# Kernel tuning notes

Hardware: AMD Instinct MI355X
Metric: run time of the kernel (lower is better)

Reference implementation:

```python
import jax, jax.numpy as jnp
import numpy as np

S, D, H = 2048, 1024, 16
DH = D // H
EPS = 1e-5


def setup_inputs() -> dict:
    key = jax.random.key(0)
    ks = jax.random.split(key, 6)
    scale = 0.02
    return {
        "inputs": jax.random.normal(ks[0], (S, D), dtype=jnp.float32),
        "ln_w": jnp.ones((D,), dtype=jnp.float32),
        "ln_b": jnp.zeros((D,), dtype=jnp.float32),
        "Wq": jax.random.normal(ks[1], (D, D), dtype=jnp.float32) * scale,
        "Wk": jax.random.normal(ks[2], (D, D), dtype=jnp.float32) * scale,
        "Wv": jax.random.normal(ks[3], (D, D), dtype=jnp.float32) * scale,
        "Wo": jax.random.normal(ks[4], (D, D), dtype=jnp.float32) * scale,
    }


def reference(inputs, ln_w, ln_b, Wq, Wk, Wv, Wo):
    # Pre-LayerNorm (per token), matching eqx.nn.LayerNorm (eps=1e-5)
    mu = jnp.mean(inputs, axis=-1, keepdims=True)
    var = jnp.var(inputs, axis=-1, keepdims=True)
    x = (inputs - mu) / jnp.sqrt(var + EPS) * ln_w + ln_b  # [S, D]

    # QKV projections (eqx Linear: y = W @ x, no bias) -> [S, H, DH]
    q = (x @ Wq.T).reshape(S, H, DH)
    k = (x @ Wk.T).reshape(S, H, DH)
    v = (x @ Wv.T).reshape(S, H, DH)

    # Scaled dot-product attention; softmax forced to full precision
    scores = jnp.einsum("shd,thd->hst", q, k) / jnp.sqrt(jnp.asarray(DH, x.dtype))
    attn = jax.nn.softmax(scores.astype(jnp.float32), axis=-1).astype(x.dtype)
    # (dropout is identity in inference mode)
    ctx = jnp.einsum("hst,thd->shd", attn, v).reshape(S, D)

    out = ctx @ Wo.T  # output projection
    # outer dropout is identity in inference mode; residual add
    return out + inputs
```

## Files before the change

### kernel.cpp

```cpp
#include <hip/hip_runtime.h>
#include <cstdint>
#include <cstddef>

typedef unsigned short u16;
typedef unsigned int u32;
typedef __attribute__((ext_vector_type(8))) short bf16x8;
typedef __attribute__((ext_vector_type(4))) short bf16x4;
typedef __attribute__((ext_vector_type(4))) float f32x4;
typedef __attribute__((ext_vector_type(4))) unsigned short u16x4;

#if __has_builtin(__builtin_amdgcn_mfma_f32_16x16x16bf16_1k)
#define MFMA16(a, b, c) __builtin_amdgcn_mfma_f32_16x16x16bf16_1k(a, b, c, 0, 0, 0)
#else
static __device__ __forceinline__ f32x4 mfma16_asm(bf16x4 a, bf16x4 b, f32x4 c) {
  asm volatile("v_mfma_f32_16x16x16_bf16 %0, %1, %2, %0\n\ts_nop 4"
               : "+v"(c) : "v"(a), "v"(b));
  return c;
}
#define MFMA16(a, b, c) mfma16_asm(a, b, c)
#endif

__device__ __forceinline__ u16 f2b(float f) {
  union { float f; unsigned u; } un; un.f = f;
  unsigned u = un.u;
  return (u16)((u + 0x7fffu + ((u >> 16) & 1u)) >> 16);
}

__device__ __forceinline__ u32 pkbf(float a, float b) {
  union { float f; u32 u; } ua, ub; ua.f = a; ub.f = b;
  return ((ua.u + 0x8000u) >> 16) | (((ub.u + 0x8000u) >> 16) << 16);
}

__device__ __forceinline__ void gload_lds16(const u16* g, u16* l) {
  __builtin_amdgcn_global_load_lds(
      (const __attribute__((address_space(1))) void*)g,
      (__attribute__((address_space(3))) void*)l, 16, 0, 0);
}

__device__ __forceinline__ void gemm128x64(
    const u16* __restrict__ A, const u16* __restrict__ B,
    u16* smA, u16* smB, int bm, int bn,
    float* outf, u16* outb, const float* __restrict__ resid, int ostride)
{
  const int tid = threadIdx.x;
  const int wave = tid >> 6, lane = tid & 63;
  const int quad = lane >> 4, l16 = lane & 15;
  const int wm = wave >> 1, wn = wave & 1;

  f32x4 acc[4][2];
  const f32x4 zero4 = {0.f, 0.f, 0.f, 0.f};
#pragma unroll
  for (int i = 0; i < 4; i++)
#pragma unroll
    for (int j = 0; j < 2; j++) acc[i][j] = zero4;

  for (int k0 = 0; k0 < 1024; k0 += 32) {
#pragma unroll
    for (int r = 0; r < 2; r++) {
      const int c = r * 256 + wave * 64 + lane;
      gload_lds16(A + (size_t)(bm * 128 + (c >> 2)) * 1024 + k0 + (c & 3) * 8,
                  smA + (size_t)(r * 256 + wave * 64) * 8);
    }
    {
      const int c = wave * 64 + lane;
      gload_lds16(B + (size_t)(bn * 64 + (c >> 2)) * 1024 + k0 + (c & 3) * 8,
                  smB + (size_t)(wave * 64) * 8);
    }
    __syncthreads();
    bf16x8 afr[4], bfr[2];
#pragma unroll
    for (int t = 0; t < 4; t++)
      afr[t] = *(const bf16x8*)(smA + (wm * 64 + t * 16 + l16) * 32 + quad * 8);
#pragma unroll
    for (int t = 0; t < 2; t++)
      bfr[t] = *(const bf16x8*)(smB + (wn * 32 + t * 16 + l16) * 32 + quad * 8);
#pragma unroll
    for (int mt = 0; mt < 4; mt++)
#pragma unroll
      for (int nt = 0; nt < 2; nt++)
        acc[mt][nt] = __builtin_amdgcn_mfma_f32_16x16x32_bf16(afr[mt], bfr[nt], acc[mt][nt], 0, 0, 0);
    __syncthreads();
  }
#pragma unroll
  for (int mt = 0; mt < 4; mt++)
#pragma unroll
    for (int nt = 0; nt < 2; nt++)
#pragma unroll
      for (int r = 0; r < 4; r++) {
        const int row = bm * 128 + wm * 64 + mt * 16 + quad * 4 + r;
        const int col = bn * 64 + wn * 32 + nt * 16 + l16;
        if (outb) outb[(size_t)row * ostride + col] = f2b(acc[mt][nt][r]);
        else outf[(size_t)row * ostride + col] =
                 acc[mt][nt][r] + resid[(size_t)row * ostride + col];
      }
}

__global__ __launch_bounds__(256, 3) void proj_k(
    const u16* __restrict__ xb, const u16* __restrict__ Wb,
    u16* __restrict__ qkbuf, u16* __restrict__ vTb)
{
  __shared__ u16 smA[128 * 32];
  __shared__ u16 smB[64 * 32];
  int b = blockIdx.x;
  const u16 *A, *B; u16* o; int bm, bn;
  if (b < 512) {
    A = xb; B = Wb; o = qkbuf; bm = b >> 5; bn = b & 31;
  } else {
    b -= 512;
    A = Wb + (size_t)2 * (1 << 20); B = xb; o = vTb; bm = b >> 5; bn = b & 31;
  }
  gemm128x64(A, B, smA, smB, bm, bn, nullptr, o, nullptr, 2048);
}

__global__ __launch_bounds__(256, 3) void out_k(
    const u16* __restrict__ ctxb, const u16* __restrict__ Wob,
    float* __restrict__ out, const float* __restrict__ x)
{
  __shared__ u16 smA[128 * 32];
  __shared__ u16 smB[64 * 32];
  gemm128x64(ctxb, Wob, smA, smB, blockIdx.y, blockIdx.x, out, nullptr, x, 1024);
}

__global__ __launch_bounds__(256) void pre_k(
    const float* __restrict__ x, const float* __restrict__ lnw, const float* __restrict__ lnb,
    const float* __restrict__ w0, const float* __restrict__ w1,
    const float* __restrict__ w2, const float* __restrict__ w3,
    u16* __restrict__ xb, u16* __restrict__ Wb)
{
  const int b = blockIdx.x;
  const int tid = threadIdx.x;
  if (b < 2048) {
    const int s = b;
    const float4 v = ((const float4*)(x + (size_t)s * 1024))[tid];
    float sum = v.x + v.y + v.z + v.w;
    float sq  = v.x * v.x + v.y * v.y + v.z * v.z + v.w * v.w;
#pragma unroll
    for (int off = 32; off >= 1; off >>= 1) {
      sum += __shfl_down(sum, off);
      sq  += __shfl_down(sq, off);
    }
    __shared__ float sS[4], sQ[4];
    const int wave = tid >> 6, lane = tid & 63;
    if (lane == 0) { sS[wave] = sum; sQ[wave] = sq; }
    __syncthreads();
    const float ts = sS[0] + sS[1] + sS[2] + sS[3];
    const float tq = sQ[0] + sQ[1] + sQ[2] + sQ[3];
    const float mu = ts * (1.0f / 1024.0f);
    const float var = tq * (1.0f / 1024.0f) - mu * mu;
    const float rstd = rsqrtf(var + 1e-5f);
    const float4 wv = ((const float4*)lnw)[tid];
    const float4 bv = ((const float4*)lnb)[tid];
    u16x4 o;
    o[0] = f2b((v.x - mu) * rstd * wv.x + bv.x);
    o[1] = f2b((v.y - mu) * rstd * wv.y + bv.y);
    o[2] = f2b((v.z - mu) * rstd * wv.z + bv.z);
    o[3] = f2b((v.w - mu) * rstd * wv.w + bv.w);
    *(u16x4*)(xb + (size_t)s * 1024 + tid * 4) = o;
  } else {
    const unsigned i = (unsigned)(b - 2048) * 1024u + tid * 4u;
    const unsigned NW = 1u << 20;
    const float* src; unsigned loc; float sc;
    if (i < NW)            { src = w0; loc = i;           sc = 0.125f; }
    else if (i < 2u * NW)  { src = w1; loc = i - NW;      sc = 1.0f; }
    else if (i < 3u * NW)  { src = w2; loc = i - 2u * NW; sc = 1.0f; }
    else                   { src = w3; loc = i - 3u * NW; sc = 1.0f; }
    const float4 v = *(const float4*)(src + loc);
    u16x4 r;
    r[0] = f2b(v.x * sc); r[1] = f2b(v.y * sc); r[2] = f2b(v.z * sc); r[3] = f2b(v.w * sc);
    *(u16x4*)(Wb + i) = r;
  }
}

__global__ __launch_bounds__(256, 2) void attn_k(
    const u16* __restrict__ qkbuf,
    const u16* __restrict__ vT,
    u16* __restrict__ ctx)
{
  const int h = blockIdx.y;
  const int q0 = blockIdx.x * 64;
  __shared__ __align__(16) unsigned char arena[65536];
  u16* kvbuf = (u16*)arena;
  const int tid = threadIdx.x;
  const int wave = tid >> 6, lane = tid & 63;
  const int quad = lane >> 4, l16 = lane & 15;
  const int a7 = l16 & 7;
  const u16* kg = qkbuf + 1024;

  bf16x8 qf[4][2];
#pragma unroll
  for (int s = 0; s < 4; s++)
#pragma unroll
    for (int ks = 0; ks < 2; ks++)
      qf[s][ks] = *(const bf16x8*)(qkbuf + (size_t)(q0 + s * 16 + l16) * 2048 + h * 64 + ks * 32 + quad * 8);

  const f32x4 zero4 = {0.f, 0.f, 0.f, 0.f};
  f32x4 Oacc[4][4];
#pragma unroll
  for (int s = 0; s < 4; s++)
#pragma unroll
    for (int dt = 0; dt < 4; dt++) Oacc[s][dt] = zero4;
  float lacc[4] = {0.f, 0.f, 0.f, 0.f};

#define STAGE(T, bf)                                                                     \
  {                                                                                      \
    _Pragma("unroll")                                                                    \
    for (int i = 0; i < 4; i++) {                                                        \
      const int idx = (wave * 4 + i) * 64 + lane;                                        \
      const int kt = idx >> 3, kc = (idx & 7) ^ (kt & 7);                                \
      gload_lds16(kg + (size_t)((T) * 128 + kt) * 2048 + h * 64 + kc * 8,                \
                  kvbuf + (bf) * 16384 + (size_t)(wave * 4 + i) * 512);                  \
      const int vd = idx >> 4, vc = (idx & 15) ^ (vd & 7);                               \
      gload_lds16(vT + (size_t)(h * 64 + vd) * 2048 + (T) * 128 + vc * 8,                \
                  kvbuf + (bf) * 16384 + 8192 + (size_t)(wave * 4 + i) * 512);           \
    }                                                                                    \
  }

  STAGE(0, 0);
  __syncthreads();

  for (int T = 0; T < 16; T++) {
    const int bf = T & 1;
    if (T + 1 < 16) STAGE(T + 1, 1 - bf);
    const u16* kb = kvbuf + bf * 16384;
    const u16* vb = kb + 8192;

    f32x4 st[2][4];
#pragma unroll
    for (int ntl = 0; ntl < 2; ntl++) {
      const int nt = wave * 2 + ntl;
      const u16* kr = kb + (nt * 16 + l16) * 64;
      const bf16x8 ka0 = *(const bf16x8*)(kr + (quad ^ a7) * 8);
      const bf16x8 ka1 = *(const bf16x8*)(kr + ((4 + quad) ^ a7) * 8);
#pragma unroll
      for (int s = 0; s < 4; s++) {
        f32x4 t0 = __builtin_amdgcn_mfma_f32_16x16x32_bf16(ka0, qf[s][0], zero4, 0, 0, 0);
        st[ntl][s] = __builtin_amdgcn_mfma_f32_16x16x32_bf16(ka1, qf[s][1], t0, 0, 0, 0);
      }
    }

    bf16x4 pk[2][4];
#pragma unroll
    for (int ntl = 0; ntl < 2; ntl++)
#pragma unroll
      for (int s = 0; s < 4; s++) {
        const float p0 = __expf(st[ntl][s][0]);
        const float p1 = __expf(st[ntl][s][1]);
        const float p2 = __expf(st[ntl][s][2]);
        const float p3 = __expf(st[ntl][s][3]);
        lacc[s] += (p0 + p1) + (p2 + p3);
        union { u32 u[2]; bf16x4 v; } pp;
        pp.u[0] = pkbf(p0, p1);
        pp.u[1] = pkbf(p2, p3);
        pk[ntl][s] = pp.v;
      }

#pragma unroll
    for (int ntl = 0; ntl < 2; ntl++)
#pragma unroll
      for (int dt = 0; dt < 4; dt++) {
        const bf16x4 bv = *(const bf16x4*)(vb + (dt * 16 + l16) * 128 +
            (((wave * 4 + ntl * 2 + (quad >> 1)) ^ a7) * 8 + (quad & 1) * 4));
#pragma unroll
        for (int s = 0; s < 4; s++)
          Oacc[s][dt] = MFMA16(pk[ntl][s], bv, Oacc[s][dt]);
      }
    __syncthreads();
  }
#undef STAGE

  float* rl = (float*)arena;
#pragma unroll
  for (int s = 0; s < 4; s++) {
    float l = lacc[s];
    l += __shfl_xor(l, 16);
    l += __shfl_xor(l, 32);
    if (quad == 0) rl[wave * 64 + s * 16 + l16] = l;
  }
  __syncthreads();
  const int m = tid >> 2, dg = (tid & 3) * 16;
  const float inv = 1.0f / (rl[m] + rl[64 + m] + rl[128 + m] + rl[192 + m]);
  __syncthreads();

  float* ro = (float*)arena;
#pragma unroll
  for (int s = 0; s < 4; s++)
#pragma unroll
    for (int dt = 0; dt < 4; dt++)
#pragma unroll
      for (int r = 0; r < 4; r++) {
        const int mr = s * 16 + quad * 4 + r;
        const int dc = (dt * 16 + l16) ^ ((mr & 7) << 1);
        ro[wave * 4096 + mr * 64 + dc] = Oacc[s][dt][r];
      }
  __syncthreads();
  u16* dst = ctx + (size_t)(q0 + m) * 1024 + h * 64 + dg;
  const int msw = (m & 7) << 1;
#pragma unroll
  for (int g = 0; g < 4; g++) {
    u16x4 o;
#pragma unroll
    for (int j = 0; j < 4; j++) {
      const int dc = (dg + g * 4 + j) ^ msw;
      const int base = m * 64 + dc;
      const float v = ro[base] + ro[4096 + base] + ro[8192 + base] + ro[12288 + base];
      o[j] = f2b(v * inv);
    }
    *(u16x4*)(dst + g * 4) = o;
  }
}

extern "C" void kernel_launch(void* const* d_in, const int* in_sizes, int n_in,
                              void* d_out, int out_size, void* d_ws, size_t ws_size,
                              hipStream_t stream)
{
  const float* x   = (const float*)d_in[0];
  const float* lnw = (const float*)d_in[1];
  const float* lnb = (const float*)d_in[2];
  const float* Wq  = (const float*)d_in[3];
  const float* Wk  = (const float*)d_in[4];
  const float* Wv  = (const float*)d_in[5];
  const float* Wo  = (const float*)d_in[6];

  u16* ws    = (u16*)d_ws;
  u16* xb    = ws;
  u16* Wb    = xb + (size_t)2048 * 1024;
  u16* qkbuf = Wb + (size_t)4 * 1024 * 1024;
  u16* vTb   = qkbuf + (size_t)2048 * 2048;
  u16* ctxb  = vTb + (size_t)1024 * 2048;

  pre_k<<<6144, 256, 0, stream>>>(x, lnw, lnb, Wq, Wk, Wv, Wo, xb, Wb);
  proj_k<<<768, 256, 0, stream>>>(xb, Wb, qkbuf, vTb);
  attn_k<<<dim3(32, 16), 256, 0, stream>>>(qkbuf, vTb, ctxb);
  out_k<<<dim3(16, 16), 256, 0, stream>>>(ctxb, Wb + (size_t)3 * (1 << 20), (float*)d_out, x);
}
```

Before: 153.3 us.

## Give each wave private LDS staging and drop block-wide barriers in GEMMs and attention

The GEMM and attention kernels now have each wave load only the A/B or K/V tiles it consumes into its own LDS region. Each wave waits on its own vmcnt and no longer hits __syncthreads every k-step. Fragments are read to registers before the next stage is issued, so a single double buffer is safe without barriers. The Q scale now folds in log2(e) so exp2f replaces __expf. The cost is that shared tiles are loaded once per wave instead of once per block, which raises global traffic and LDS use, and out_k occupancy drops from 3 to 2 blocks.

```diff
diff --git a/kernel.cpp b/kernel.cpp
--- a/kernel.cpp
+++ b/kernel.cpp
@@ -20,6 +20,8 @@
 #define MFMA16(a, b, c) mfma16_asm(a, b, c)
 #endif
 
+#define VMWAIT0() asm volatile("s_waitcnt vmcnt(0)" ::: "memory")
+
 __device__ __forceinline__ u16 f2b(float f) {
   union { float f; unsigned u; } un; un.f = f;
   unsigned u = un.u;
@@ -37,88 +39,113 @@
       (__attribute__((address_space(3))) void*)l, 16, 0, 0);
 }
 
-__device__ __forceinline__ void gemm128x64(
-    const u16* __restrict__ A, const u16* __restrict__ B,
-    u16* smA, u16* smB, int bm, int bn,
-    float* outf, u16* outb, const float* __restrict__ resid, int ostride)
-{
+#define GEMM_STAGE(ks, bfi)                                                               \
+  {                                                                                       \
+    const int k0g = (ks) * 32;                                                            \
+    u16* ad = (u16*)(wbase + (bfi) * 4096);                                               \
+    u16* bd = (u16*)(wbase + 8192 + (bfi) * 2048);                                        \
+    _Pragma("unroll")                                                                     \
+    for (int i = 0; i < 4; i++)                                                           \
+      gload_lds16(Ag + (size_t)(am0 + i * 16 + (lane >> 2)) * 1024 + k0g + (lane & 3) * 8,\
+                  ad + i * 512);                                                          \
+    _Pragma("unroll")                                                                     \
+    for (int i = 0; i < 2; i++)                                                           \
+      gload_lds16(Bg + (size_t)(bn0 + i * 16 + (lane >> 2)) * 1024 + k0g + (lane & 3) * 8,\
+                  bd + i * 512);                                                          \
+  }
+
+#define GEMM_BODY()                                                                       \
+  f32x4 acc[4][2];                                                                        \
+  {                                                                                       \
+    const f32x4 zero4 = {0.f, 0.f, 0.f, 0.f};                                             \
+    _Pragma("unroll")                                                                     \
+    for (int i = 0; i < 4; i++)                                                           \
+      _Pragma("unroll")                                                                   \
+      for (int j = 0; j < 2; j++) acc[i][j] = zero4;                                      \
+  }                                                                                       \
+  GEMM_STAGE(0, 0);                                                                       \
+  for (int ks = 0; ks < 32; ks++) {                                                       \
+    const int bfi = ks & 1;                                                               \
+    const u16* aw = (const u16*)(wbase + bfi * 4096);                                     \
+    const u16* bw = (const u16*)(wbase + 8192 + bfi * 2048);                              \
+    VMWAIT0();                                                                            \
+    bf16x8 afr[4], bfr[2];                                                                \
+    _Pragma("unroll")                                                                     \
+    for (int t = 0; t < 4; t++)                                                           \
+      afr[t] = *(const bf16x8*)(aw + (t * 16 + l16) * 32 + quad * 8);                     \
+    _Pragma("unroll")                                                                     \
+    for (int t = 0; t < 2; t++)                                                           \
+      bfr[t] = *(const bf16x8*)(bw + (t * 16 + l16) * 32 + quad * 8);                     \
+    if (ks + 1 < 32) GEMM_STAGE(ks + 1, 1 - bfi);                                         \
+    _Pragma("unroll")                                                                     \
+    for (int mt = 0; mt < 4; mt++)                                                        \
+      _Pragma("unroll")                                                                   \
+      for (int nt = 0; nt < 2; nt++)                                                      \
+        acc[mt][nt] = __builtin_amdgcn_mfma_f32_16x16x32_bf16(afr[mt], bfr[nt],           \
+                                                              acc[mt][nt], 0, 0, 0);     \
+  }
+
+__global__ __launch_bounds__(256, 3) void proj_k(
+    const u16* __restrict__ xb, const u16* __restrict__ Wb,
+    u16* __restrict__ qkbuf, u16* __restrict__ vTb)
+{
+  __shared__ __align__(16) unsigned char garena[49152];
   const int tid = threadIdx.x;
   const int wave = tid >> 6, lane = tid & 63;
   const int quad = lane >> 4, l16 = lane & 15;
   const int wm = wave >> 1, wn = wave & 1;
-
-  f32x4 acc[4][2];
-  const f32x4 zero4 = {0.f, 0.f, 0.f, 0.f};
-#pragma unroll
-  for (int i = 0; i < 4; i++)
-#pragma unroll
-    for (int j = 0; j < 2; j++) acc[i][j] = zero4;
-
-  for (int k0 = 0; k0 < 1024; k0 += 32) {
-#pragma unroll
-    for (int r = 0; r < 2; r++) {
-      const int c = r * 256 + wave * 64 + lane;
-      gload_lds16(A + (size_t)(bm * 128 + (c >> 2)) * 1024 + k0 + (c & 3) * 8,
-                  smA + (size_t)(r * 256 + wave * 64) * 8);
-    }
-    {
-      const int c = wave * 64 + lane;
-      gload_lds16(B + (size_t)(bn * 64 + (c >> 2)) * 1024 + k0 + (c & 3) * 8,
-                  smB + (size_t)(wave * 64) * 8);
-    }
-    __syncthreads();
-    bf16x8 afr[4], bfr[2];
-#pragma unroll
-    for (int t = 0; t < 4; t++)
-      afr[t] = *(const bf16x8*)(smA + (wm * 64 + t * 16 + l16) * 32 + quad * 8);
-#pragma unroll
-    for (int t = 0; t < 2; t++)
-      bfr[t] = *(const bf16x8*)(smB + (wn * 32 + t * 16 + l16) * 32 + quad * 8);
-#pragma unroll
-    for (int mt = 0; mt < 4; mt++)
-#pragma unroll
-      for (int nt = 0; nt < 2; nt++)
-        acc[mt][nt] = __builtin_amdgcn_mfma_f32_16x16x32_bf16(afr[mt], bfr[nt], acc[mt][nt], 0, 0, 0);
-    __syncthreads();
-  }
+  unsigned char* wbase = garena + wave * 12288;
+
+  int b = blockIdx.x;
+  const u16 *Ag, *Bg; u16* o; int bm, bn;
+  if (b < 512) { Ag = xb; Bg = Wb; o = qkbuf; bm = b >> 5; bn = b & 31; }
+  else { b -= 512; Ag = Wb + (size_t)2 * (1 << 20); Bg = xb; o = vTb; bm = b >> 5; bn = b & 31; }
+  const int am0 = bm * 128 + wm * 64;
+  const int bn0 = bn * 64 + wn * 32;
+
+  GEMM_BODY();
+
 #pragma unroll
   for (int mt = 0; mt < 4; mt++)
 #pragma unroll
     for (int nt = 0; nt < 2; nt++)
 #pragma unroll
       for (int r = 0; r < 4; r++) {
-        const int row = bm * 128 + wm * 64 + mt * 16 + quad * 4 + r;
-        const int col = bn * 64 + wn * 32 + nt * 16 + l16;
-        if (outb) outb[(size_t)row * ostride + col] = f2b(acc[mt][nt][r]);
-        else outf[(size_t)row * ostride + col] =
-                 acc[mt][nt][r] + resid[(size_t)row * ostride + col];
-      }
-}
-
-__global__ __launch_bounds__(256, 3) void proj_k(
-    const u16* __restrict__ xb, const u16* __restrict__ Wb,
-    u16* __restrict__ qkbuf, u16* __restrict__ vTb)
-{
-  __shared__ u16 smA[128 * 32];
-  __shared__ u16 smB[64 * 32];
-  int b = blockIdx.x;
-  const u16 *A, *B; u16* o; int bm, bn;
-  if (b < 512) {
-    A = xb; B = Wb; o = qkbuf; bm = b >> 5; bn = b & 31;
-  } else {
-    b -= 512;
-    A = Wb + (size_t)2 * (1 << 20); B = xb; o = vTb; bm = b >> 5; bn = b & 31;
-  }
-  gemm128x64(A, B, smA, smB, bm, bn, nullptr, o, nullptr, 2048);
-}
-
-__global__ __launch_bounds__(256, 3) void out_k(
+        const int row = am0 + mt * 16 + quad * 4 + r;
+        const int col = bn0 + nt * 16 + l16;
+        o[(size_t)row * 2048 + col] = f2b(acc[mt][nt][r]);
+      }
+}
+
+__global__ __launch_bounds__(256, 2) void out_k(
     const u16* __restrict__ ctxb, const u16* __restrict__ Wob,
     float* __restrict__ out, const float* __restrict__ x)
 {
-  __shared__ u16 smA[128 * 32];
-  __shared__ u16 smB[64 * 32];
-  gemm128x64(ctxb, Wob, smA, smB, blockIdx.y, blockIdx.x, out, nullptr, x, 1024);
+  __shared__ __align__(16) unsigned char garena[49152];
+  const int tid = threadIdx.x;
+  const int wave = tid >> 6, lane = tid & 63;
+  const int quad = lane >> 4, l16 = lane & 15;
+  const int wm = wave >> 1, wn = wave & 1;
+  unsigned char* wbase = garena + wave * 12288;
+
+  const u16* Ag = ctxb;
+  const u16* Bg = Wob;
+  const int am0 = blockIdx.y * 128 + wm * 64;
+  const int bn0 = blockIdx.x * 64 + wn * 32;
+
+  GEMM_BODY();
+
+#pragma unroll
+  for (int mt = 0; mt < 4; mt++)
+#pragma unroll
+    for (int nt = 0; nt < 2; nt++)
+#pragma unroll
+      for (int r = 0; r < 4; r++) {
+        const int row = am0 + mt * 16 + quad * 4 + r;
+        const int col = bn0 + nt * 16 + l16;
+        out[(size_t)row * 1024 + col] =
+            acc[mt][nt][r] + x[(size_t)row * 1024 + col];
+      }
 }
 
 __global__ __launch_bounds__(256) void pre_k(
@@ -160,7 +187,7 @@
     const unsigned i = (unsigned)(b - 2048) * 1024u + tid * 4u;
     const unsigned NW = 1u << 20;
     const float* src; unsigned loc; float sc;
-    if (i < NW)            { src = w0; loc = i;           sc = 0.125f; }
+    if (i < NW)            { src = w0; loc = i;           sc = 0.125f * 1.44269504f; }
     else if (i < 2u * NW)  { src = w1; loc = i - NW;      sc = 1.0f; }
     else if (i < 3u * NW)  { src = w2; loc = i - 2u * NW; sc = 1.0f; }
     else                   { src = w3; loc = i - 3u * NW; sc = 1.0f; }
@@ -179,12 +206,12 @@
   const int h = blockIdx.y;
   const int q0 = blockIdx.x * 64;
   __shared__ __align__(16) unsigned char arena[65536];
-  u16* kvbuf = (u16*)arena;
   const int tid = threadIdx.x;
   const int wave = tid >> 6, lane = tid & 63;
   const int quad = lane >> 4, l16 = lane & 15;
   const int a7 = l16 & 7;
   const u16* kg = qkbuf + 1024;
+  unsigned char* wb8 = arena + wave * 16384;
 
   bf16x8 qf[4][2];
 #pragma unroll
@@ -201,52 +228,67 @@
     for (int dt = 0; dt < 4; dt++) Oacc[s][dt] = zero4;
   float lacc[4] = {0.f, 0.f, 0.f, 0.f};
 
-#define STAGE(T, bf)                                                                     \
-  {                                                                                      \
-    _Pragma("unroll")                                                                    \
-    for (int i = 0; i < 4; i++) {                                                        \
-      const int idx = (wave * 4 + i) * 64 + lane;                                        \
-      const int kt = idx >> 3, kc = (idx & 7) ^ (kt & 7);                                \
-      gload_lds16(kg + (size_t)((T) * 128 + kt) * 2048 + h * 64 + kc * 8,                \
-                  kvbuf + (bf) * 16384 + (size_t)(wave * 4 + i) * 512);                  \
-      const int vd = idx >> 4, vc = (idx & 15) ^ (vd & 7);                               \
-      gload_lds16(vT + (size_t)(h * 64 + vd) * 2048 + (T) * 128 + vc * 8,                \
-                  kvbuf + (bf) * 16384 + 8192 + (size_t)(wave * 4 + i) * 512);           \
-    }                                                                                    \
-  }
-
-  STAGE(0, 0);
-  __syncthreads();
+#define STAGEW(T, bfi)                                                                    \
+  {                                                                                       \
+    u16* kd = (u16*)(wb8 + (bfi) * 4096);                                                 \
+    u16* vd_ = (u16*)(wb8 + 8192 + (bfi) * 4096);                                         \
+    _Pragma("unroll")                                                                     \
+    for (int i = 0; i < 4; i++) {                                                         \
+      gload_lds16(kg + (size_t)((T) * 128 + wave * 32 + i * 8 + (lane >> 3)) * 2048 +     \
+                      h * 64 + (((lane & 7) ^ ((lane >> 3) & 7)) * 8),                    \
+                  kd + i * 512);                                                          \
+      gload_lds16(vT + (size_t)(h * 64 + ((lane - 2 * i) & 63)) * 2048 +                  \
+                      (T) * 128 + wave * 32 + i * 8,                                      \
+                  vd_ + i * 512);                                                         \
+    }                                                                                     \
+  }
+
+  STAGEW(0, 0);
 
   for (int T = 0; T < 16; T++) {
     const int bf = T & 1;
-    if (T + 1 < 16) STAGE(T + 1, 1 - bf);
-    const u16* kb = kvbuf + bf * 16384;
-    const u16* vb = kb + 8192;
+    const u16* kb = (const u16*)(wb8 + bf * 4096);
+    const u16* vb = (const u16*)(wb8 + 8192 + bf * 4096);
+
+    VMWAIT0();
+
+    bf16x8 ka0[2], ka1[2];
+#pragma unroll
+    for (int ntl = 0; ntl < 2; ntl++) {
+      const int lt = ntl * 16 + l16;
+      ka0[ntl] = *(const bf16x8*)(kb + lt * 64 + (quad ^ a7) * 8);
+      ka1[ntl] = *(const bf16x8*)(kb + lt * 64 + ((4 + quad) ^ a7) * 8);
+    }
+    bf16x4 bv[2][4];
+#pragma unroll
+    for (int ntl = 0; ntl < 2; ntl++) {
+      const int c = ntl * 2 + (quad >> 1);
+#pragma unroll
+      for (int dt = 0; dt < 4; dt++)
+        bv[ntl][dt] = *(const bf16x4*)(vb + (c * 64 + ((dt * 16 + l16 + 2 * c) & 63)) * 8 +
+                                       (quad & 1) * 4);
+    }
+
+    if (T + 1 < 16) STAGEW(T + 1, 1 - bf);
 
     f32x4 st[2][4];
 #pragma unroll
-    for (int ntl = 0; ntl < 2; ntl++) {
-      const int nt = wave * 2 + ntl;
-      const u16* kr = kb + (nt * 16 + l16) * 64;
-      const bf16x8 ka0 = *(const bf16x8*)(kr + (quad ^ a7) * 8);
-      const bf16x8 ka1 = *(const bf16x8*)(kr + ((4 + quad) ^ a7) * 8);
+    for (int ntl = 0; ntl < 2; ntl++)
 #pragma unroll
       for (int s = 0; s < 4; s++) {
-        f32x4 t0 = __builtin_amdgcn_mfma_f32_16x16x32_bf16(ka0, qf[s][0], zero4, 0, 0, 0);
-        st[ntl][s] = __builtin_amdgcn_mfma_f32_16x16x32_bf16(ka1, qf[s][1], t0, 0, 0, 0);
-      }
-    }
+        f32x4 t0 = __builtin_amdgcn_mfma_f32_16x16x32_bf16(ka0[ntl], qf[s][0], zero4, 0, 0, 0);
+        st[ntl][s] = __builtin_amdgcn_mfma_f32_16x16x32_bf16(ka1[ntl], qf[s][1], t0, 0, 0, 0);
+      }
 
     bf16x4 pk[2][4];
 #pragma unroll
     for (int ntl = 0; ntl < 2; ntl++)
 #pragma unroll
       for (int s = 0; s < 4; s++) {
-        const float p0 = __expf(st[ntl][s][0]);
-        const float p1 = __expf(st[ntl][s][1]);
-        const float p2 = __expf(st[ntl][s][2]);
-        const float p3 = __expf(st[ntl][s][3]);
+        const float p0 = exp2f(st[ntl][s][0]);
+        const float p1 = exp2f(st[ntl][s][1]);
+        const float p2 = exp2f(st[ntl][s][2]);
+        const float p3 = exp2f(st[ntl][s][3]);
         lacc[s] += (p0 + p1) + (p2 + p3);
         union { u32 u[2]; bf16x4 v; } pp;
         pp.u[0] = pkbf(p0, p1);
@@ -257,16 +299,14 @@
 #pragma unroll
     for (int ntl = 0; ntl < 2; ntl++)
 #pragma unroll
-      for (int dt = 0; dt < 4; dt++) {
-        const bf16x4 bv = *(const bf16x4*)(vb + (dt * 16 + l16) * 128 +
-            (((wave * 4 + ntl * 2 + (quad >> 1)) ^ a7) * 8 + (quad & 1) * 4));
+      for (int dt = 0; dt < 4; dt++)
 #pragma unroll
         for (int s = 0; s < 4; s++)
-          Oacc[s][dt] = MFMA16(pk[ntl][s], bv, Oacc[s][dt]);
-      }
-    __syncthreads();
-  }
-#undef STAGE
+          Oacc[s][dt] = MFMA16(pk[ntl][s], bv[ntl][dt], Oacc[s][dt]);
+  }
+#undef STAGEW
+
+  __syncthreads();
 
   float* rl = (float*)arena;
 #pragma unroll
```

Result: slower. 161.1 us (+5.1%).

## Split attention KV range across two blocks and combine partials in separate kernel

Applied to the files above, without the earlier changes.

Attention now runs with a z dimension of 2. Each block processes half of the key sequence in 64-key tiles using half the LDS, and writes unnormalized fp32 partial outputs and row sums to workspace. A new combine kernel adds the two partials, normalizes them and writes the bf16 context. The Q weight is pre-scaled by log2(e) so exp2f can replace __expf, and occupancy is raised to 4 blocks per CU. The aim is more parallelism and occupancy in attention, paid for by extra fp32 partial traffic and an extra launch. The old out_k is kept but unused, and out2_k replaces it.

```diff
diff --git a/kernel.cpp b/kernel.cpp
--- a/kernel.cpp
+++ b/kernel.cpp
@@ -113,6 +113,15 @@
 }
 
 __global__ __launch_bounds__(256, 3) void out_k(
+    const u16* __restrict__ ctxb, const u16* __restrict__ Wob,
+    float* __restrict__ out, const float* __restrict__ x)
+{
+  __shared__ u16 smA[128 * 32];
+  __shared__ u16 smB[64 * 32];
+  gemm128x64(ctxb, Wob, smA, smB, blockIdx.y, blockIdx.x, nullptr, nullptr, x, 1024);
+}
+
+__global__ __launch_bounds__(256, 3) void out2_k(
     const u16* __restrict__ ctxb, const u16* __restrict__ Wob,
     float* __restrict__ out, const float* __restrict__ x)
 {
@@ -160,7 +169,7 @@
     const unsigned i = (unsigned)(b - 2048) * 1024u + tid * 4u;
     const unsigned NW = 1u << 20;
     const float* src; unsigned loc; float sc;
-    if (i < NW)            { src = w0; loc = i;           sc = 0.125f; }
+    if (i < NW)            { src = w0; loc = i;           sc = 0.125f * 1.44269504f; }
     else if (i < 2u * NW)  { src = w1; loc = i - NW;      sc = 1.0f; }
     else if (i < 3u * NW)  { src = w2; loc = i - 2u * NW; sc = 1.0f; }
     else                   { src = w3; loc = i - 3u * NW; sc = 1.0f; }
@@ -171,15 +180,16 @@
   }
 }
 
-__global__ __launch_bounds__(256, 2) void attn_k(
+__global__ __launch_bounds__(256, 4) void attn_k(
     const u16* __restrict__ qkbuf,
     const u16* __restrict__ vT,
-    u16* __restrict__ ctx)
+    float* __restrict__ pO,
+    float* __restrict__ pL)
 {
   const int h = blockIdx.y;
   const int q0 = blockIdx.x * 64;
-  __shared__ __align__(16) unsigned char arena[65536];
-  u16* kvbuf = (u16*)arena;
+  const int z = blockIdx.z;
+  __shared__ __align__(16) unsigned char arena[32768];
   const int tid = threadIdx.x;
   const int wave = tid >> 6, lane = tid & 63;
   const int quad = lane >> 4, l16 = lane & 15;
@@ -201,18 +211,21 @@
     for (int dt = 0; dt < 4; dt++) Oacc[s][dt] = zero4;
   float lacc[4] = {0.f, 0.f, 0.f, 0.f};
 
-#define STAGE(T, bf)                                                                     \
-  {                                                                                      \
-    _Pragma("unroll")                                                                    \
-    for (int i = 0; i < 4; i++) {                                                        \
-      const int idx = (wave * 4 + i) * 64 + lane;                                        \
-      const int kt = idx >> 3, kc = (idx & 7) ^ (kt & 7);                                \
-      gload_lds16(kg + (size_t)((T) * 128 + kt) * 2048 + h * 64 + kc * 8,                \
-                  kvbuf + (bf) * 16384 + (size_t)(wave * 4 + i) * 512);                  \
-      const int vd = idx >> 4, vc = (idx & 15) ^ (vd & 7);                               \
-      gload_lds16(vT + (size_t)(h * 64 + vd) * 2048 + (T) * 128 + vc * 8,                \
-                  kvbuf + (bf) * 16384 + 8192 + (size_t)(wave * 4 + i) * 512);           \
-    }                                                                                    \
+#define STAGE(T, bfi)                                                                     \
+  {                                                                                       \
+    const int t0 = z * 1024 + (T) * 64;                                                   \
+    u16* kd = (u16*)(arena + (bfi) * 16384);                                              \
+    u16* vdst = (u16*)(arena + (bfi) * 16384 + 8192);                                     \
+    _Pragma("unroll")                                                                     \
+    for (int i = 0; i < 2; i++) {                                                         \
+      const int idx = (i * 4 + wave) * 64 + lane;                                         \
+      const int kt = idx >> 3, kc = (idx & 7) ^ (kt & 7);                                 \
+      gload_lds16(kg + (size_t)(t0 + kt) * 2048 + h * 64 + kc * 8,                        \
+                  kd + (size_t)(i * 4 + wave) * 512);                                     \
+      const int vd = idx >> 3, vc = (idx & 7) ^ (vd & 7);                                 \
+      gload_lds16(vT + (size_t)(h * 64 + vd) * 2048 + t0 + vc * 8,                        \
+                  vdst + (size_t)(i * 4 + wave) * 512);                                   \
+    }                                                                                     \
   }
 
   STAGE(0, 0);
@@ -221,92 +234,113 @@
   for (int T = 0; T < 16; T++) {
     const int bf = T & 1;
     if (T + 1 < 16) STAGE(T + 1, 1 - bf);
-    const u16* kb = kvbuf + bf * 16384;
-    const u16* vb = kb + 8192;
-
-    f32x4 st[2][4];
-#pragma unroll
-    for (int ntl = 0; ntl < 2; ntl++) {
-      const int nt = wave * 2 + ntl;
-      const u16* kr = kb + (nt * 16 + l16) * 64;
-      const bf16x8 ka0 = *(const bf16x8*)(kr + (quad ^ a7) * 8);
-      const bf16x8 ka1 = *(const bf16x8*)(kr + ((4 + quad) ^ a7) * 8);
-#pragma unroll
-      for (int s = 0; s < 4; s++) {
-        f32x4 t0 = __builtin_amdgcn_mfma_f32_16x16x32_bf16(ka0, qf[s][0], zero4, 0, 0, 0);
-        st[ntl][s] = __builtin_amdgcn_mfma_f32_16x16x32_bf16(ka1, qf[s][1], t0, 0, 0, 0);
-      }
-    }
-
-    bf16x4 pk[2][4];
-#pragma unroll
-    for (int ntl = 0; ntl < 2; ntl++)
-#pragma unroll
-      for (int s = 0; s < 4; s++) {
-        const float p0 = __expf(st[ntl][s][0]);
-        const float p1 = __expf(st[ntl][s][1]);
-        const float p2 = __expf(st[ntl][s][2]);
-        const float p3 = __expf(st[ntl][s][3]);
-        lacc[s] += (p0 + p1) + (p2 + p3);
-        union { u32 u[2]; bf16x4 v; } pp;
-        pp.u[0] = pkbf(p0, p1);
-        pp.u[1] = pkbf(p2, p3);
-        pk[ntl][s] = pp.v;
-      }
-
-#pragma unroll
-    for (int ntl = 0; ntl < 2; ntl++)
-#pragma unroll
-      for (int dt = 0; dt < 4; dt++) {
-        const bf16x4 bv = *(const bf16x4*)(vb + (dt * 16 + l16) * 128 +
-            (((wave * 4 + ntl * 2 + (quad >> 1)) ^ a7) * 8 + (quad & 1) * 4));
-#pragma unroll
-        for (int s = 0; s < 4; s++)
-          Oacc[s][dt] = MFMA16(pk[ntl][s], bv, Oacc[s][dt]);
-      }
+    const u16* kb = (const u16*)(arena + bf * 16384);
+    const u16* vb = (const u16*)(arena + bf * 16384 + 8192);
+
+    const int krow = (wave * 16 + l16) * 64;
+    const bf16x8 ka0 = *(const bf16x8*)(kb + krow + (quad ^ a7) * 8);
+    const bf16x8 ka1 = *(const bf16x8*)(kb + krow + ((4 + quad) ^ a7) * 8);
+    bf16x4 bv[4];
+#pragma unroll
+    for (int dt = 0; dt < 4; dt++)
+      bv[dt] = *(const bf16x4*)(vb + (dt * 16 + l16) * 64 +
+                                ((wave * 2 + (quad >> 1)) ^ a7) * 8 + (quad & 1) * 4);
+
+    f32x4 st[4];
+#pragma unroll
+    for (int s = 0; s < 4; s++) {
+      f32x4 t0v = __builtin_amdgcn_mfma_f32_16x16x32_bf16(ka0, qf[s][0], zero4, 0, 0, 0);
+      st[s] = __builtin_amdgcn_mfma_f32_16x16x32_bf16(ka1, qf[s][1], t0v, 0, 0, 0);
+    }
+
+    bf16x4 pk[4];
+#pragma unroll
+    for (int s = 0; s < 4; s++) {
+      const float p0 = exp2f(st[s][0]);
+      const float p1 = exp2f(st[s][1]);
+      const float p2 = exp2f(st[s][2]);
+      const float p3 = exp2f(st[s][3]);
+      lacc[s] += (p0 + p1) + (p2 + p3);
+      union { u32 u[2]; bf16x4 v; } pp;
+      pp.u[0] = pkbf(p0, p1);
+      pp.u[1] = pkbf(p2, p3);
+      pk[s] = pp.v;
+    }
+
+#pragma unroll
+    for (int dt = 0; dt < 4; dt++)
+#pragma unroll
+      for (int s = 0; s < 4; s++)
+        Oacc[s][dt] = MFMA16(pk[s], bv[dt], Oacc[s][dt]);
+
     __syncthreads();
   }
 #undef STAGE
 
-  float* rl = (float*)arena;
+  float* lds_l = (float*)arena;
 #pragma unroll
   for (int s = 0; s < 4; s++) {
     float l = lacc[s];
     l += __shfl_xor(l, 16);
     l += __shfl_xor(l, 32);
-    if (quad == 0) rl[wave * 64 + s * 16 + l16] = l;
+    if (quad == 0) lds_l[wave * 64 + s * 16 + l16] = l;
   }
   __syncthreads();
-  const int m = tid >> 2, dg = (tid & 3) * 16;
-  const float inv = 1.0f / (rl[m] + rl[64 + m] + rl[128 + m] + rl[192 + m]);
+  if (tid < 64) {
+    const float lt = lds_l[tid] + lds_l[64 + tid] + lds_l[128 + tid] + lds_l[192 + tid];
+    pL[((size_t)z * 2048 + q0 + tid) * 16 + h] = lt;
+  }
   __syncthreads();
 
   float* ro = (float*)arena;
-#pragma unroll
-  for (int s = 0; s < 4; s++)
-#pragma unroll
-    for (int dt = 0; dt < 4; dt++)
-#pragma unroll
-      for (int r = 0; r < 4; r++) {
-        const int mr = s * 16 + quad * 4 + r;
-        const int dc = (dt * 16 + l16) ^ ((mr & 7) << 1);
-        ro[wave * 4096 + mr * 64 + dc] = Oacc[s][dt][r];
-      }
-  __syncthreads();
-  u16* dst = ctx + (size_t)(q0 + m) * 1024 + h * 64 + dg;
-  const int msw = (m & 7) << 1;
-#pragma unroll
-  for (int g = 0; g < 4; g++) {
-    u16x4 o;
-#pragma unroll
-    for (int j = 0; j < 4; j++) {
-      const int dc = (dg + g * 4 + j) ^ msw;
-      const int base = m * 64 + dc;
-      const float v = ro[base] + ro[4096 + base] + ro[8192 + base] + ro[12288 + base];
-      o[j] = f2b(v * inv);
-    }
-    *(u16x4*)(dst + g * 4) = o;
-  }
+  const int m = tid >> 2, cg = (tid & 3) * 8;
+#pragma unroll
+  for (int dh = 0; dh < 2; dh++) {
+#pragma unroll
+    for (int s = 0; s < 4; s++)
+#pragma unroll
+      for (int dtl = 0; dtl < 2; dtl++)
+#pragma unroll
+        for (int r = 0; r < 4; r++) {
+          const int mr = s * 16 + quad * 4 + r;
+          const int dc = (dtl * 16 + l16) ^ ((mr & 7) << 1) ^ (((mr >> 2) & 1) << 4);
+          ro[wave * 2048 + mr * 32 + dc] = Oacc[s][dh * 2 + dtl][r];
+        }
+    __syncthreads();
+    float v[8];
+#pragma unroll
+    for (int j = 0; j < 8; j++) {
+      const int dc = (cg + j) ^ ((m & 7) << 1) ^ (((m >> 2) & 1) << 4);
+      const int base = m * 32 + dc;
+      v[j] = ro[base] + ro[2048 + base] + ro[4096 + base] + ro[6144 + base];
+    }
+    float* dst = pO + ((size_t)z * 2048 + q0 + m) * 1024 + h * 64 + dh * 32 + cg;
+    *(float4*)dst = make_float4(v[0], v[1], v[2], v[3]);
+    *(float4*)(dst + 4) = make_float4(v[4], v[5], v[6], v[7]);
+    __syncthreads();
+  }
+}
+
+__global__ __launch_bounds__(256) void comb_k(
+    const float* __restrict__ pO, const float* __restrict__ pL, u16* __restrict__ ctx)
+{
+  const unsigned ci = blockIdx.x * 256u + threadIdx.x;
+  const unsigned row = ci >> 7, col8 = (ci & 127u) * 8u;
+  const unsigned hh = col8 >> 6;
+  const float l = pL[row * 16 + hh] + pL[2048 * 16 + row * 16 + hh];
+  const float inv = 1.0f / l;
+  const float* a = pO + (size_t)row * 1024 + col8;
+  const float* b = pO + (size_t)2048 * 1024 + (size_t)row * 1024 + col8;
+  const float4 a0 = *(const float4*)a, a1 = *(const float4*)(a + 4);
+  const float4 b0 = *(const float4*)b, b1 = *(const float4*)(b + 4);
+  u16x4 o0, o1;
+  o0[0] = f2b((a0.x + b0.x) * inv); o0[1] = f2b((a0.y + b0.y) * inv);
+  o0[2] = f2b((a0.z + b0.z) * inv); o0[3] = f2b((a0.w + b0.w) * inv);
+  o1[0] = f2b((a1.x + b1.x) * inv); o1[1] = f2b((a1.y + b1.y) * inv);
+  o1[2] = f2b((a1.z + b1.z) * inv); o1[3] = f2b((a1.w + b1.w) * inv);
+  u16* d = ctx + (size_t)row * 1024 + col8;
+  *(u16x4*)d = o0;
+  *(u16x4*)(d + 4) = o1;
 }
 
 extern "C" void kernel_launch(void* const* d_in, const int* in_sizes, int n_in,
@@ -327,9 +361,12 @@
   u16* qkbuf = Wb + (size_t)4 * 1024 * 1024;
   u16* vTb   = qkbuf + (size_t)2048 * 2048;
   u16* ctxb  = vTb + (size_t)1024 * 2048;
+  float* pO  = (float*)(ctxb + (size_t)2048 * 1024);
+  float* pL  = pO + (size_t)2 * 2048 * 1024;
 
   pre_k<<<6144, 256, 0, stream>>>(x, lnw, lnb, Wq, Wk, Wv, Wo, xb, Wb);
   proj_k<<<768, 256, 0, stream>>>(xb, Wb, qkbuf, vTb);
-  attn_k<<<dim3(32, 16), 256, 0, stream>>>(qkbuf, vTb, ctxb);
-  out_k<<<dim3(16, 16), 256, 0, stream>>>(ctxb, Wb + (size_t)3 * (1 << 20), (float*)d_out, x);
-}
+  attn_k<<<dim3(32, 16, 2), 256, 0, stream>>>(qkbuf, vTb, pO, pL);
+  comb_k<<<1024, 256, 0, stream>>>(pO, pL, ctxb);
+  out2_k<<<dim3(16, 16), 256, 0, stream>>>(ctxb, Wb + (size_t)3 * (1 << 20), (float*)d_out, x);
+}
```

Result: slower. 198.5 us (+29.5%).

## Load K and V fragments straight from global into registers in attention

Applied to the files above, without the earlier changes.

The attention kernel no longer stages K and V tiles through double-buffered shared memory with async global-to-LDS copies and per-tile barriers. Each wave now reads its own K fragments and V^T fragments directly from global memory into registers, prefetching the next tile's K one step ahead, and the per-iteration __syncthreads is removed. Separately, the log2(e) factor is folded into the Q weight scale so the softmax can use exp2f instead of __expf. This trades LDS traffic and barriers for uncoalesced, cache-dependent global loads and V loads with less latency hiding.

```diff
diff --git a/kernel.cpp b/kernel.cpp
--- a/kernel.cpp
+++ b/kernel.cpp
@@ -112,7 +112,7 @@
   gemm128x64(A, B, smA, smB, bm, bn, nullptr, o, nullptr, 2048);
 }
 
-__global__ __launch_bounds__(256, 3) void out_k(
+__global__ __launch_bounds__(256, 3) void out2_k(
     const u16* __restrict__ ctxb, const u16* __restrict__ Wob,
     float* __restrict__ out, const float* __restrict__ x)
 {
@@ -160,7 +160,7 @@
     const unsigned i = (unsigned)(b - 2048) * 1024u + tid * 4u;
     const unsigned NW = 1u << 20;
     const float* src; unsigned loc; float sc;
-    if (i < NW)            { src = w0; loc = i;           sc = 0.125f; }
+    if (i < NW)            { src = w0; loc = i;           sc = 0.125f * 1.44269504f; }
     else if (i < 2u * NW)  { src = w1; loc = i - NW;      sc = 1.0f; }
     else if (i < 3u * NW)  { src = w2; loc = i - 2u * NW; sc = 1.0f; }
     else                   { src = w3; loc = i - 3u * NW; sc = 1.0f; }
@@ -179,12 +179,9 @@
   const int h = blockIdx.y;
   const int q0 = blockIdx.x * 64;
   __shared__ __align__(16) unsigned char arena[65536];
-  u16* kvbuf = (u16*)arena;
   const int tid = threadIdx.x;
   const int wave = tid >> 6, lane = tid & 63;
   const int quad = lane >> 4, l16 = lane & 15;
-  const int a7 = l16 & 7;
-  const u16* kg = qkbuf + 1024;
 
   bf16x8 qf[4][2];
 #pragma unroll
@@ -201,72 +198,80 @@
     for (int dt = 0; dt < 4; dt++) Oacc[s][dt] = zero4;
   float lacc[4] = {0.f, 0.f, 0.f, 0.f};
 
-#define STAGE(T, bf)                                                                     \
-  {                                                                                      \
-    _Pragma("unroll")                                                                    \
-    for (int i = 0; i < 4; i++) {                                                        \
-      const int idx = (wave * 4 + i) * 64 + lane;                                        \
-      const int kt = idx >> 3, kc = (idx & 7) ^ (kt & 7);                                \
-      gload_lds16(kg + (size_t)((T) * 128 + kt) * 2048 + h * 64 + kc * 8,                \
-                  kvbuf + (bf) * 16384 + (size_t)(wave * 4 + i) * 512);                  \
-      const int vd = idx >> 4, vc = (idx & 15) ^ (vd & 7);                               \
-      gload_lds16(vT + (size_t)(h * 64 + vd) * 2048 + (T) * 128 + vc * 8,                \
-                  kvbuf + (bf) * 16384 + 8192 + (size_t)(wave * 4 + i) * 512);           \
-    }                                                                                    \
-  }
-
-  STAGE(0, 0);
+  const u16* kbase = qkbuf + 1024 + (size_t)(wave * 32 + l16) * 2048 + h * 64 + quad * 8;
+  const u16* vbase = vT + (size_t)(h * 64 + l16) * 2048 + wave * 32 + quad * 4;
+
+  bf16x8 ka0[2][2], ka1[2][2];
+
+#define LOADK(T, pb)                                                        \
+  {                                                                         \
+    _Pragma("unroll")                                                       \
+    for (int ntl = 0; ntl < 2; ntl++) {                                     \
+      const u16* kr = kbase + (size_t)((T) * 128 + ntl * 16) * 2048;        \
+      ka0[pb][ntl] = *(const bf16x8*)(kr);                                  \
+      ka1[pb][ntl] = *(const bf16x8*)(kr + 32);                             \
+    }                                                                       \
+  }
+
+#define COMPUTE(T, pb)                                                      \
+  {                                                                         \
+                        \
+    bf16x4 bvv[2][4];                                                       \
+    _Pragma("unroll")                                                       \
+    for (int ntl = 0; ntl < 2; ntl++)                                       \
+      _Pragma("unroll")                                                     \
+      for (int dt = 0; dt < 4; dt++)                                        \
+        bvv[ntl][dt] = *(const bf16x4*)(vbase + (size_t)dt * 16 * 2048 +    \
+                                        (T) * 128 + ntl * 16);              \
+                                          \
+    if ((T) + 1 < 16) LOADK((T) + 1, 1 - (pb));                             \
+            \
+    f32x4 st[2][4];                                                         \
+    _Pragma("unroll")                                                       \
+    for (int ntl = 0; ntl < 2; ntl++)                                       \
+      _Pragma("unroll")                                                     \
+      for (int s = 0; s < 4; s++) {                                         \
+        f32x4 t0v = __builtin_amdgcn_mfma_f32_16x16x32_bf16(                \
+            ka0[pb][ntl], qf[s][0], zero4, 0, 0, 0);                        \
+        st[ntl][s] = __builtin_amdgcn_mfma_f32_16x16x32_bf16(               \
+            ka1[pb][ntl], qf[s][1], t0v, 0, 0, 0);                          \
+      }                                                                     \
+                               \
+    bf16x4 pk[2][4];                                                        \
+    _Pragma("unroll")                                                       \
+    for (int ntl = 0; ntl < 2; ntl++)                                       \
+      _Pragma("unroll")                                                     \
+      for (int s = 0; s < 4; s++) {                                         \
+        const float p0 = exp2f(st[ntl][s][0]);                              \
+        const float p1 = exp2f(st[ntl][s][1]);                              \
+        const float p2 = exp2f(st[ntl][s][2]);                              \
+        const float p3 = exp2f(st[ntl][s][3]);                              \
+        lacc[s] += (p0 + p1) + (p2 + p3);                                   \
+        union { u32 u[2]; bf16x4 v; } pp;                                   \
+        pp.u[0] = pkbf(p0, p1);                                             \
+        pp.u[1] = pkbf(p2, p3);                                             \
+        pk[ntl][s] = pp.v;                                                  \
+      }                                                                     \
+                                   \
+    _Pragma("unroll")                                                       \
+    for (int ntl = 0; ntl < 2; ntl++)                                       \
+      _Pragma("unroll")                                                     \
+      for (int dt = 0; dt < 4; dt++)                                        \
+        _Pragma("unroll")                                                   \
+        for (int s = 0; s < 4; s++)                                         \
+          Oacc[s][dt] = MFMA16(pk[ntl][s], bvv[ntl][dt], Oacc[s][dt]);      \
+  }
+
+  LOADK(0, 0);
+#pragma unroll 1
+  for (int T = 0; T < 16; T += 2) {
+    COMPUTE(T, 0);
+    COMPUTE(T + 1, 1);
+  }
+#undef LOADK
+#undef COMPUTE
+
   __syncthreads();
-
-  for (int T = 0; T < 16; T++) {
-    const int bf = T & 1;
-    if (T + 1 < 16) STAGE(T + 1, 1 - bf);
-    const u16* kb = kvbuf + bf * 16384;
-    const u16* vb = kb + 8192;
-
-    f32x4 st[2][4];
-#pragma unroll
-    for (int ntl = 0; ntl < 2; ntl++) {
-      const int nt = wave * 2 + ntl;
-      const u16* kr = kb + (nt * 16 + l16) * 64;
-      const bf16x8 ka0 = *(const bf16x8*)(kr + (quad ^ a7) * 8);
-      const bf16x8 ka1 = *(const bf16x8*)(kr + ((4 + quad) ^ a7) * 8);
-#pragma unroll
-      for (int s = 0; s < 4; s++) {
-        f32x4 t0 = __builtin_amdgcn_mfma_f32_16x16x32_bf16(ka0, qf[s][0], zero4, 0, 0, 0);
-        st[ntl][s] = __builtin_amdgcn_mfma_f32_16x16x32_bf16(ka1, qf[s][1], t0, 0, 0, 0);
-      }
-    }
-
-    bf16x4 pk[2][4];
-#pragma unroll
-    for (int ntl = 0; ntl < 2; ntl++)
-#pragma unroll
-      for (int s = 0; s < 4; s++) {
-        const float p0 = __expf(st[ntl][s][0]);
-        const float p1 = __expf(st[ntl][s][1]);
-        const float p2 = __expf(st[ntl][s][2]);
-        const float p3 = __expf(st[ntl][s][3]);
-        lacc[s] += (p0 + p1) + (p2 + p3);
-        union { u32 u[2]; bf16x4 v; } pp;
-        pp.u[0] = pkbf(p0, p1);
-        pp.u[1] = pkbf(p2, p3);
-        pk[ntl][s] = pp.v;
-      }
-
-#pragma unroll
-    for (int ntl = 0; ntl < 2; ntl++)
-#pragma unroll
-      for (int dt = 0; dt < 4; dt++) {
-        const bf16x4 bv = *(const bf16x4*)(vb + (dt * 16 + l16) * 128 +
-            (((wave * 4 + ntl * 2 + (quad >> 1)) ^ a7) * 8 + (quad & 1) * 4));
-#pragma unroll
-        for (int s = 0; s < 4; s++)
-          Oacc[s][dt] = MFMA16(pk[ntl][s], bv, Oacc[s][dt]);
-      }
-    __syncthreads();
-  }
-#undef STAGE
 
   float* rl = (float*)arena;
 #pragma unroll
@@ -331,5 +336,5 @@
   pre_k<<<6144, 256, 0, stream>>>(x, lnw, lnb, Wq, Wk, Wv, Wo, xb, Wb);
   proj_k<<<768, 256, 0, stream>>>(xb, Wb, qkbuf, vTb);
   attn_k<<<dim3(32, 16), 256, 0, stream>>>(qkbuf, vTb, ctxb);
-  out_k<<<dim3(16, 16), 256, 0, stream>>>(ctxb, Wb + (size_t)3 * (1 << 20), (float*)d_out, x);
-}
+  out2_k<<<dim3(16, 16), 256, 0, stream>>>(ctxb, Wb + (size_t)3 * (1 << 20), (float*)d_out, x);
+}
```

Result: slower. 171.9 us (+12.1%).
